# Kernel tuning notes

Hardware: AMD Instinct MI355X
Metric: run time of the kernel (lower is better)

Reference implementation:

```python
import jax, jax.numpy as jnp
import numpy as np

KS = 3
N = KS ** 3  # 27 kernel sample points


def conv3d(x, w, b=None, pad=1):
    out = jax.lax.conv_general_dilated(
        x, w, (1, 1, 1), [(pad, pad)] * 3,
        dimension_numbers=('NCDHW', 'OIDHW', 'NCDHW'))
    if b is not None:
        out = out + b[None, :, None, None, None]
    return out


def batchnorm(x, g, b, eps=1e-5):
    # training-mode BN: batch statistics over (N,D,H,W), biased variance (torch default)
    m = x.mean(axis=(0, 2, 3, 4), keepdims=True)
    v = x.var(axis=(0, 2, 3, 4), keepdims=True)
    return (x - m) * jax.lax.rsqrt(v + eps) * g[None, :, None, None, None] + b[None, :, None, None, None]


def deform_conv3d(x, offset, w, pad=1):
    # x: (b,c,D,H,W); offset: (b,3N,D,H,W) channel order [d-offsets | h-offsets | w-offsets]
    b, c, D, H, W = x.shape
    xp = jnp.pad(x, ((0, 0), (0, 0), (pad, pad), (pad, pad), (pad, pad)))
    Dp, Hp, Wp = D + 2 * pad, H + 2 * pad, W + 2 * pad
    dt = offset.dtype
    r = (jnp.arange(KS) - (KS - 1) // 2).astype(dt)
    pn = jnp.stack(jnp.meshgrid(r, r, r, indexing='ij'), -1).reshape(N, 3)  # kernel grid offsets
    base = jnp.stack(jnp.meshgrid(jnp.arange(D) + pad, jnp.arange(H) + pad,
                                  jnp.arange(W) + pad, indexing='ij'), -1).astype(dt)  # (D,H,W,3)
    off = jnp.transpose(offset.reshape(b, 3, N, D, H, W), (0, 3, 4, 5, 2, 1))  # (b,D,H,W,N,3)
    p = base[None, :, :, :, None, :] + pn[None, None, None, None] + off  # fractional sample coords
    dims = jnp.array([Dp, Hp, Wp], dtype=dt)
    q0 = jnp.floor(p)
    q0c = jnp.clip(q0, 0, dims - 1)
    q1c = jnp.clip(q0 + 1, 0, dims - 1)
    pc = jnp.clip(p, 0, dims - 1)
    wlo = 1.0 + (q0c - pc)  # per-axis trilinear weight, low corner
    whi = 1.0 - (q1c - pc)  # per-axis trilinear weight, high corner
    q0i = q0c.astype(jnp.int32)
    q1i = q1c.astype(jnp.int32)
    xpf = xp.reshape(b, c, -1)
    M = D * H * W * N
    acc = jnp.zeros((b, c, D, H, W, N), dtype=x.dtype)
    for corner in range(8):  # fixed 8 trilinear corners
        sel = [(corner >> a) & 1 for a in range(3)]
        q = [q1i[..., a] if sel[a] else q0i[..., a] for a in range(3)]
        g = (whi[..., 0] if sel[0] else wlo[..., 0]) \
            * (whi[..., 1] if sel[1] else wlo[..., 1]) \
            * (whi[..., 2] if sel[2] else wlo[..., 2])
        idx = (q[0] * Hp + q[1]) * Wp + q[2]  # (b,D,H,W,N) flat gather index
        vals = jnp.take_along_axis(
            xpf, jnp.broadcast_to(idx.reshape(b, 1, M), (b, c, M)), axis=2
        ).reshape(b, c, D, H, W, N)
        acc = acc + g[:, None] * vals
    # kernel-stride-KS conv over the reshaped blocks == contraction over (c, N)
    outc = w.shape[0]
    return jnp.einsum('bcdhwn,ocn->bodhw', acc, w.reshape(outc, c, N))


def setup_inputs():
    key = jax.random.key(0)
    ks = jax.random.split(key, 8)
    f32 = jnp.float32
    return {
        'x': jax.random.normal(ks[0], (16, 1, 28, 28, 28), f32),
        'off_w': jax.random.normal(ks[1], (81, 1, 3, 3, 3), f32) * 0.05,
        'off_b': jnp.zeros((81,), f32),
        'dconv_w': jax.random.normal(ks[2], (32, 1, 3, 3, 3), f32) * 0.2,
        'bn1_g': jnp.ones((32,), f32), 'bn1_b': jnp.zeros((32,), f32),
        'conv2_w': jax.random.normal(ks[3], (64, 32, 3, 3, 3), f32) * 0.06,
        'conv2_b': jnp.zeros((64,), f32),
        'bn2_g': jnp.ones((64,), f32), 'bn2_b': jnp.zeros((64,), f32),
        'conv3_w': jax.random.normal(ks[4], (128, 64, 3, 3, 3), f32) * 0.04,
        'conv3_b': jnp.zeros((128,), f32),
        'bn3_g': jnp.ones((128,), f32), 'bn3_b': jnp.zeros((128,), f32),
        'conv4_w': jax.random.normal(ks[5], (128, 128, 3, 3, 3), f32) * 0.03,
        'conv4_b': jnp.zeros((128,), f32),
        'bn4_g': jnp.ones((128,), f32), 'bn4_b': jnp.zeros((128,), f32),
        'fc_w': jax.random.normal(ks[6], (10, 128), f32) * 0.1,
        'fc_b': jnp.zeros((10,), f32),
    }


def reference(x, off_w, off_b, dconv_w, bn1_g, bn1_b, conv2_w, conv2_b, bn2_g, bn2_b,
              conv3_w, conv3_b, bn3_g, bn3_b, conv4_w, conv4_b, bn4_g, bn4_b, fc_w, fc_b):
    offsets = conv3d(x, off_w, off_b)  # (b,81,D,H,W)
    h = batchnorm(jax.nn.relu(deform_conv3d(x, offsets, dconv_w)), bn1_g, bn1_b)
    h = batchnorm(jax.nn.relu(conv3d(h, conv2_w, conv2_b)), bn2_g, bn2_b)
    h = batchnorm(jax.nn.relu(conv3d(h, conv3_w, conv3_b)), bn3_g, bn3_b)
    h = batchnorm(jax.nn.relu(conv3d(h, conv4_w, conv4_b)), bn4_g, bn4_b)
    h = h.mean(axis=(2, 3, 4))  # avg_pool3d over full (28,28,d) -> (b,128)
    logits = h @ fc_w.T + fc_b
    return jax.nn.log_softmax(logits, axis=1), offsets
```

## Files before the change

kernel.cpp:

```cpp
#include <hip/hip_runtime.h>
#include <math.h>

#define Sv 21952
#define HWc 784
#define CNT 351232.0f
#define EPS 1e-5f
#define PV 27000
#define PT (16 * PV)

typedef short bf16x8 __attribute__((ext_vector_type(8)));
typedef float f32x4 __attribute__((ext_vector_type(4)));
typedef float f32x16 __attribute__((ext_vector_type(16)));
typedef unsigned short u16x8 __attribute__((ext_vector_type(8)));

__device__ __forceinline__ unsigned short f2bf(float f) {
    unsigned u = __float_as_uint(f);
    u = (u + 0x7FFFu + ((u >> 16) & 1u)) >> 16;
    return (unsigned short)u;
}
__device__ __forceinline__ float bf2f(unsigned short h) {
    return __uint_as_float(((unsigned)h) << 16);
}

__device__ __forceinline__ void async16(const unsigned short* g, unsigned short* l) {
    __builtin_amdgcn_global_load_lds(
        (const __attribute__((address_space(1))) unsigned int*)g,
        (__attribute__((address_space(3))) unsigned int*)l, 16, 0, 0);
}

__global__ __launch_bounds__(256) void k_offsets(const float* __restrict__ x,
        const float* __restrict__ ow, const float* __restrict__ ob,
        float* __restrict__ out) {
    __shared__ float w_s[81 * 27];
    __shared__ float b_s[81];
    for (int i = threadIdx.x; i < 81 * 27; i += 256) w_s[i] = ow[i];
    if (threadIdx.x < 81) b_s[threadIdx.x] = ob[threadIdx.x];
    __syncthreads();
    int idx = blockIdx.x * 256 + threadIdx.x;
    int n = idx / Sv, s = idx % Sv;
    int d = s / HWc, r = s % HWc, h = r / 28, w = r % 28;
    const float* xb = x + (long)n * Sv;
    float xv[27];
    #pragma unroll
    for (int dz = 0; dz < 3; dz++)
      #pragma unroll
      for (int dy = 0; dy < 3; dy++)
        #pragma unroll
        for (int dx = 0; dx < 3; dx++) {
            int zz = d + dz - 1, yy = h + dy - 1, xx = w + dx - 1;
            bool ok = (unsigned)zz < 28u && (unsigned)yy < 28u && (unsigned)xx < 28u;
            xv[dz * 9 + dy * 3 + dx] = ok ? xb[zz * HWc + yy * 28 + xx] : 0.f;
        }
    float* op = out + (long)n * 81 * Sv + s;
    for (int c = 0; c < 81; c++) {
        float acc = b_s[c];
        #pragma unroll
        for (int k = 0; k < 27; k++) acc += xv[k] * w_s[c * 27 + k];
        op[(long)c * Sv] = acc;
    }
}

__device__ __forceinline__ float fetch_pad(const float* __restrict__ xb,
                                           int zq, int yq, int xq) {
    int z = zq - 1, y = yq - 1, xx = xq - 1;
    bool ok = (unsigned)z < 28u && (unsigned)y < 28u && (unsigned)xx < 28u;
    return ok ? xb[z * HWc + y * 28 + xx] : 0.f;
}

__global__ __launch_bounds__(256) void k_deform(const float* __restrict__ x,
        const float* __restrict__ off, const float* __restrict__ dw,
        unsigned short* __restrict__ h1p) {
    __shared__ float w_s[32 * 27];
    for (int i = threadIdx.x; i < 32 * 27; i += 256) w_s[i] = dw[i];
    __syncthreads();
    int idx = blockIdx.x * 256 + threadIdx.x;
    int n = idx / Sv, s = idx % Sv;
    int d = s / HWc, r = s % HWc, h = r / 28, w = r % 28;
    const float* xb = x + (long)n * Sv;
    const float* ofb = off + (long)n * 81 * Sv + s;
    float v[27];
    #pragma unroll
    for (int k = 0; k < 27; k++) {
        int ki = k / 9, kj = (k / 3) % 3, kl = k % 3;
        float pd = (float)(d + ki) + ofb[(long)k * Sv];
        float ph = (float)(h + kj) + ofb[(long)(27 + k) * Sv];
        float pw = (float)(w + kl) + ofb[(long)(54 + k) * Sv];
        float q0d = floorf(pd), q0h = floorf(ph), q0w = floorf(pw);
        float pcd = fminf(fmaxf(pd, 0.f), 29.f);
        float pch = fminf(fmaxf(ph, 0.f), 29.f);
        float pcw = fminf(fmaxf(pw, 0.f), 29.f);
        float q0cd = fminf(fmaxf(q0d, 0.f), 29.f);
        float q0ch = fminf(fmaxf(q0h, 0.f), 29.f);
        float q0cw = fminf(fmaxf(q0w, 0.f), 29.f);
        float q1cd = fminf(fmaxf(q0d + 1.f, 0.f), 29.f);
        float q1ch = fminf(fmaxf(q0h + 1.f, 0.f), 29.f);
        float q1cw = fminf(fmaxf(q0w + 1.f, 0.f), 29.f);
        float wz[2] = {1.f + (q0cd - pcd), 1.f - (q1cd - pcd)};
        float wy[2] = {1.f + (q0ch - pch), 1.f - (q1ch - pch)};
        float wx[2] = {1.f + (q0cw - pcw), 1.f - (q1cw - pcw)};
        int qz[2] = {(int)q0cd, (int)q1cd};
        int qy[2] = {(int)q0ch, (int)q1ch};
        int qx[2] = {(int)q0cw, (int)q1cw};
        float val = 0.f;
        #pragma unroll
        for (int cz = 0; cz < 2; cz++)
          #pragma unroll
          for (int cy = 0; cy < 2; cy++)
            #pragma unroll
            for (int cx = 0; cx < 2; cx++)
                val += wz[cz] * wy[cy] * wx[cx] * fetch_pad(xb, qz[cz], qy[cy], qx[cx]);
        v[k] = val;
    }
    unsigned pb = ((((unsigned)n * 30 + (d + 1)) * 30 + (h + 1)) * 30 + (w + 1)) * 32;
    unsigned short tmp[32];
    #pragma unroll
    for (int o = 0; o < 32; o++) {
        float acc = 0.f;
        #pragma unroll
        for (int k = 0; k < 27; k++) acc += v[k] * w_s[o * 27 + k];
        tmp[o] = f2bf(fmaxf(acc, 0.f));
    }
    u16x8* dst = (u16x8*)(h1p + pb);
    #pragma unroll
    for (int q = 0; q < 4; q++) dst[q] = ((u16x8*)tmp)[q];
}

template<int C>
__global__ __launch_bounds__(256) void k_stats_p(const unsigned short* __restrict__ buf,
        float* __restrict__ sums) {
    constexpr int G = C / 8;
    constexpr int P = 256 / G;
    int t = threadIdx.x;
    int oct = t % G, ps = t / G;
    float s1[8], s2[8];
    #pragma unroll
    for (int j = 0; j < 8; j++) { s1[j] = 0.f; s2[j] = 0.f; }
    for (int p = blockIdx.x * P + ps; p < PT; p += gridDim.x * P) {
        u16x8 v = *(const u16x8*)(buf + (long)p * C + oct * 8);
        #pragma unroll
        for (int j = 0; j < 8; j++) {
            float f = bf2f(v[j]);
            s1[j] += f; s2[j] += f * f;
        }
    }
    __shared__ float sh[2][C];
    if (t < C) { sh[0][t] = 0.f; sh[1][t] = 0.f; }
    __syncthreads();
    #pragma unroll
    for (int j = 0; j < 8; j++) {
        atomicAdd(&sh[0][oct * 8 + j], s1[j]);
        atomicAdd(&sh[1][oct * 8 + j], s2[j]);
    }
    __syncthreads();
    if (t < C) { atomicAdd(&sums[t], sh[0][t]); atomicAdd(&sums[C + t], sh[1][t]); }
}

__global__ void k_finalize(const float* __restrict__ sums, const float* __restrict__ g,
        const float* __restrict__ bb, float* __restrict__ aff, int C) {
    int c = threadIdx.x;
    if (c < C) {
        float mean = sums[c] * (1.f / CNT);
        float var = sums[C + c] * (1.f / CNT) - mean * mean;
        float a = g[c] * rsqrtf(var + EPS);
        aff[c] = a;
        aff[C + c] = bb[c] - mean * a;
    }
}

template<int CI, int COT>
__global__ __launch_bounds__(256) void k_wfrag32(const float* __restrict__ w,
        const float* __restrict__ affa, unsigned short* __restrict__ wf) {
    constexpr int NT32 = COT / 32;
    constexpr int KC = CI / 32;
    int tid = blockIdx.x * 256 + threadIdx.x;
    int lane = tid & 63, rest = tid >> 6;
    int kh = rest & 1; rest >>= 1;
    int nt = rest % NT32; rest /= NT32;
    int kc = rest % KC;
    int tap = rest / KC;
    if (tap >= 27) return;
    int co = nt * 32 + (lane & 31);
    int hi = lane >> 5;
    unsigned short tmp[8];
    #pragma unroll
    for (int j = 0; j < 8; j++) {
        int ci = kc * 32 + kh * 16 + hi * 8 + j;
        tmp[j] = f2bf(w[((long)co * CI + ci) * 27 + tap] * affa[ci]);
    }
    long oidx = ((((long)kc * 27 + tap) * NT32 + nt) * 2 + kh) * 512 + lane * 8;
    *(u16x8*)(wf + oidx) = *(u16x8*)tmp;
}

template<int CI, int COT>
__global__ __launch_bounds__(256) void k_tapsum(const float* __restrict__ w,
        const float* __restrict__ affb, float* __restrict__ S) {
    __shared__ float acc[27];
    int co = blockIdx.x;
    int t = threadIdx.x;
    if (t < 27) acc[t] = 0.f;
    __syncthreads();
    const float* wr = w + (long)co * CI * 27;
    for (int idx = t; idx < CI * 27; idx += 256)
        atomicAdd(&acc[idx % 27], wr[idx] * affb[idx / 27]);
    __syncthreads();
    if (t < 27) S[t * COT + co] = acc[t];
}

template<int COT>
__global__ void k_btab2(const float* __restrict__ S, const float* __restrict__ bias,
        float* __restrict__ T) {
    int tid = blockIdx.x * 256 + threadIdx.x;
    if (tid >= 27 * COT) return;
    int co = tid % COT, cls = tid / COT;
    int xc = cls % 3, yc = (cls / 3) % 3, zc = cls / 9;
    float val = bias[co];
    #pragma unroll
    for (int t = 0; t < 27; t++) {
        int dx = t % 3, dy = (t / 3) % 3, dz = t / 9;
        bool ok = (zc == 1 || (zc == 0 && dz >= 1) || (zc == 2 && dz <= 1))
               && (yc == 1 || (yc == 0 && dy >= 1) || (yc == 2 && dy <= 1))
               && (xc == 1 || (xc == 0 && dx >= 1) || (xc == 2 && dx <= 1));
        if (ok) val += S[t * COT + co];
    }
    T[cls * COT + co] = val;
}

template<int CI, int COT, int WN, bool PAD_OUT>
__global__ __launch_bounds__(WN * 128, 2) void k_conv_mfma(
        const unsigned short* __restrict__ in,
        const unsigned short* __restrict__ wfrag,
        const float* __restrict__ Ttab,
        unsigned short* __restrict__ out) {
    constexpr int KC = CI / 32;
    constexpr int NT32 = COT / 32;
    constexpr int NW = WN * 2;
    constexpr int NTW = (NW >= 4) ? NT32 / 2 : NT32;
    constexpr int NT = WN * 128;
    constexpr int CP = 720;
    constexpr int CUU = CP * 5;
    constexpr int NLOAD = (CUU + NT - 1) / NT;
    constexpr int LDSU = CUU + 48;
    __shared__ unsigned short lds[LDSU * 8];

    int tid = threadIdx.x, wv = tid >> 6, lane = tid & 63;
    int lcol = lane & 31, hi = lane >> 5;
    int wv_m = wv & 1, wv_n = wv >> 1;

    int bx = blockIdx.x;
    int xcd = bx & 7, loc = bx >> 3;
    int n = xcd * 2 + loc / 98;
    int rem = loc % 98;
    int z0 = (rem / 7) * 2;
    int y0 = (rem % 7) * 4;
    const unsigned short* src = in + ((long)((n * 30 + z0) * 30 + y0) * 30) * CI;

    int baseA[4];
    #pragma unroll
    for (int mt = 0; mt < 4; mt++) {
        int x = lcol; if (x > 27) x = 27;
        int pos = (wv_m * 6 + mt) * 30 + x;
        baseA[mt] = pos * 80 + hi * 16;
    }

    f32x16 acc[4][NTW];
    #pragma unroll
    for (int mt = 0; mt < 4; mt++)
        #pragma unroll
        for (int nt = 0; nt < NTW; nt++)
            #pragma unroll
            for (int e = 0; e < 16; e++) acc[mt][nt][e] = 0.f;

    for (int kc = 0; kc < KC; kc++) {
        if (kc) __syncthreads();
        #pragma unroll
        for (int j = 0; j < NLOAD; j++) {
            int wb = j * NT + (wv << 6);
            if (wb < CUU) {
                int u = wb + lane;
                if (u >= CUU) u = CUU - 1;
                int p = u / 5, s = u - p * 5;
                int q = s & 3;
                int zl = p / 180, r = p - zl * 180;
                int yl = r / 30, xl = r - yl * 30;
                int so = (zl * 900 + yl * 30 + xl) * CI + q * 8 + kc * 32;
                async16(src + so, lds + (wb << 3));
            }
        }
        __syncthreads();
        const unsigned short* pwk =
            wfrag + (long)(kc * 27) * NT32 * 1024 + (long)wv_n * (NTW * 1024)
                  + lane * 8;
        bf16x8 bc[NTW][2];
        #pragma unroll
        for (int nt = 0; nt < NTW; nt++)
            #pragma unroll
            for (int kh = 0; kh < 2; kh++)
                bc[nt][kh] = *(const bf16x8*)(pwk + nt * 1024 + kh * 512);
        #pragma unroll
        for (int tap = 0; tap < 27; tap++) {
            int td = (((tap / 9) * 6 + (tap % 9) / 3) * 30 + tap % 3) * 80;
            bf16x8 bn[NTW][2];
            if (tap < 26) {
                const unsigned short* pwn = pwk + (long)(tap + 1) * NT32 * 1024;
                #pragma unroll
                for (int nt = 0; nt < NTW; nt++)
                    #pragma unroll
                    for (int kh = 0; kh < 2; kh++)
                        bn[nt][kh] = *(const bf16x8*)(pwn + nt * 1024 + kh * 512);
            }
            bf16x8 a[2][4];
            #pragma unroll
            for (int kh = 0; kh < 2; kh++)
                #pragma unroll
                for (int mt = 0; mt < 4; mt++)
                    a[kh][mt] = *(const bf16x8*)((const char*)lds
                                 + baseA[mt] + td + kh * 32);
            #pragma unroll
            for (int kh = 0; kh < 2; kh++)
                #pragma unroll
                for (int mt = 0; mt < 4; mt++)
                    #pragma unroll
                    for (int nt = 0; nt < NTW; nt++)
                        acc[mt][nt] = __builtin_amdgcn_mfma_f32_32x32x16_bf16(
                            a[kh][mt], bc[nt][kh], acc[mt][nt], 0, 0, 0);
            if (tap < 26) {
                #pragma unroll
                for (int nt = 0; nt < NTW; nt++)
                    #pragma unroll
                    for (int kh = 0; kh < 2; kh++)
                        bc[nt][kh] = bn[nt][kh];
            }
        }
    }

    int zz = z0 + wv_m;
    int zc = (zz == 0) ? 0 : ((zz == 27) ? 2 : 1);
    #pragma unroll
    for (int mt = 0; mt < 4; mt++) {
        int y = y0 + mt;
        int yc = (y == 0) ? 0 : ((y == 27) ? 2 : 1);
        #pragma unroll
        for (int reg = 0; reg < 16; reg++) {
            int x = (reg & 3) + 8 * (reg >> 2) + 4 * hi;
            if (x >= 28) continue;
            int xc = (x == 0) ? 0 : ((x == 27) ? 2 : 1);
            int cls = (zc * 3 + yc) * 3 + xc;
            long ob;
            if (PAD_OUT)
                ob = ((long)((n * 30 + zz + 1) * 30 + y + 1) * 30 + x + 1) * COT;
            else
                ob = ((long)n * Sv + zz * HWc + y * 28 + x) * COT;
            #pragma unroll
            for (int nt = 0; nt < NTW; nt++) {
                int co = wv_n * (NTW * 32) + nt * 32 + lcol;
                float v = acc[mt][nt][reg] + Ttab[cls * COT + co];
                out[ob + co] = f2bf(fmaxf(v, 0.f));
            }
        }
    }
}

__global__ __launch_bounds__(256) void k_stats4(const unsigned short* __restrict__ h4,
        float* __restrict__ pooled, float* __restrict__ chsq) {
    int n = blockIdx.x, zs = blockIdx.y;
    int t = threadIdx.x;
    int oct = t % 16, ps = t / 16;
    long base = (long)n * Sv + zs * HWc;
    float s1[8], s2[8];
    #pragma unroll
    for (int j = 0; j < 8; j++) { s1[j] = 0.f; s2[j] = 0.f; }
    for (int p = ps; p < HWc; p += 16) {
        u16x8 v = *(const u16x8*)(h4 + (base + p) * 128 + oct * 8);
        #pragma unroll
        for (int j = 0; j < 8; j++) {
            float f = bf2f(v[j]);
            s1[j] += f; s2[j] += f * f;
        }
    }
    __shared__ float sh[2][128];
    if (t < 128) { sh[0][t] = 0.f; sh[1][t] = 0.f; }
    __syncthreads();
    #pragma unroll
    for (int j = 0; j < 8; j++) {
        atomicAdd(&sh[0][oct * 8 + j], s1[j]);
        atomicAdd(&sh[1][oct * 8 + j], s2[j]);
    }
    __syncthreads();
    if (t < 128) {
        atomicAdd(&pooled[n * 128 + t], sh[0][t]);
        atomicAdd(&chsq[t], sh[1][t]);
    }
}

__global__ __launch_bounds__(256) void k_head(const float* __restrict__ pooled,
        const float* __restrict__ chsq, const float* __restrict__ g4,
        const float* __restrict__ b4, const float* __restrict__ fcw,
        const float* __restrict__ fcb, float* __restrict__ out) {
    __shared__ float feat[16 * 128];
    __shared__ float lg[160];
    __shared__ float corr[16];
    int t = threadIdx.x;
    if (t < 128) {
        float sum = 0.f;
        for (int n = 0; n < 16; n++) sum += pooled[n * 128 + t];
        float mean = sum * (1.f / CNT);
        float var = chsq[t] * (1.f / CNT) - mean * mean;
        float a = g4[t] * rsqrtf(var + EPS);
        float bb = b4[t] - mean * a;
        for (int n = 0; n < 16; n++)
            feat[n * 128 + t] = a * (pooled[n * 128 + t] * (1.f / (float)Sv)) + bb;
    }
    __syncthreads();
    if (t < 160) {
        int n = t / 10, j = t % 10;
        float acc = fcb[j];
        for (int c = 0; c < 128; c++) acc += feat[n * 128 + c] * fcw[j * 128 + c];
        lg[t] = acc;
    }
    __syncthreads();
    if (t < 16) {
        float mx = -1e30f;
        for (int j = 0; j < 10; j++) mx = fmaxf(mx, lg[t * 10 + j]);
        float se = 0.f;
        for (int j = 0; j < 10; j++) se += expf(lg[t * 10 + j] - mx);
        corr[t] = mx + logf(se);
    }
    __syncthreads();
    if (t < 160) out[t] = lg[t] - corr[t / 10];
}

#define OFF_H3P 0L
#define OFF_H2P 110592000L
#define OFF_H1P 165888000L
#define OFF_H4  110592000L
#define OFF_WF2 200507392L
#define OFF_WF3 200617984L
#define OFF_WF4 201060352L
#define OFF_STATS 201945088L

extern "C" void kernel_launch(void* const* d_in, const int* in_sizes, int n_in,
                              void* d_out, int out_size, void* d_ws, size_t ws_size,
                              hipStream_t stream) {
    const float* x       = (const float*)d_in[0];
    const float* off_w   = (const float*)d_in[1];
    const float* off_b   = (const float*)d_in[2];
    const float* dconv_w = (const float*)d_in[3];
    const float* bn1_g   = (const float*)d_in[4];
    const float* bn1_b   = (const float*)d_in[5];
    const float* conv2_w = (const float*)d_in[6];
    const float* conv2_b = (const float*)d_in[7];
    const float* bn2_g   = (const float*)d_in[8];
    const float* bn2_b   = (const float*)d_in[9];
    const float* conv3_w = (const float*)d_in[10];
    const float* conv3_b = (const float*)d_in[11];
    const float* bn3_g   = (const float*)d_in[12];
    const float* bn3_b   = (const float*)d_in[13];
    const float* conv4_w = (const float*)d_in[14];
    const float* conv4_b = (const float*)d_in[15];
    const float* bn4_g   = (const float*)d_in[16];
    const float* bn4_b   = (const float*)d_in[17];
    const float* fc_w    = (const float*)d_in[18];
    const float* fc_b    = (const float*)d_in[19];

    float* out = (float*)d_out;
    float* offsets = out + 160;

    char* ws = (char*)d_ws;
    unsigned short* h3p = (unsigned short*)(ws + OFF_H3P);
    unsigned short* h2p = (unsigned short*)(ws + OFF_H2P);
    unsigned short* h1p = (unsigned short*)(ws + OFF_H1P);
    unsigned short* h4  = (unsigned short*)(ws + OFF_H4);
    unsigned short* wf2 = (unsigned short*)(ws + OFF_WF2);
    unsigned short* wf3 = (unsigned short*)(ws + OFF_WF3);
    unsigned short* wf4 = (unsigned short*)(ws + OFF_WF4);
    float* st = (float*)(ws + OFF_STATS);
    float* sums1 = st;        float* aff1 = st + 64;
    float* sums2 = st + 128;  float* aff2 = st + 256;
    float* sums3 = st + 384;  float* aff3 = st + 640;
    float* chsq4 = st + 896;  float* pooled = st + 1024;
    float* T2 = st + 4096;    float* T3 = st + 8192;   float* T4 = st + 16384;
    float* Sb = st + 20480;

    hipMemsetAsync(st, 0, 3072 * sizeof(float), stream);
    hipMemsetAsync(h1p, 0, 27648000L, stream);
    hipMemsetAsync(h2p, 0, 55296000L, stream);
    hipMemsetAsync(h3p, 0, 110592000L, stream);

    k_offsets<<<dim3(1372), 256, 0, stream>>>(x, off_w, off_b, offsets);
    k_deform<<<dim3(1372), 256, 0, stream>>>(x, offsets, dconv_w, h1p);

    k_stats_p<32><<<dim3(432), 256, 0, stream>>>(h1p, sums1);
    k_finalize<<<1, 32, 0, stream>>>(sums1, bn1_g, bn1_b, aff1, 32);
    k_wfrag32<32, 64><<<dim3(27), 256, 0, stream>>>(conv2_w, aff1, wf2);
    k_tapsum<32, 64><<<dim3(64), 256, 0, stream>>>(conv2_w, aff1 + 32, Sb);
    k_btab2<64><<<dim3(7), 256, 0, stream>>>(Sb, conv2_b, T2);
    k_conv_mfma<32, 64, 2, true><<<dim3(1568), 256, 0, stream>>>(h1p, wf2, T2, h2p);

    k_stats_p<64><<<dim3(432), 256, 0, stream>>>(h2p, sums2);
    k_finalize<<<1, 64, 0, stream>>>(sums2, bn2_g, bn2_b, aff2, 64);
    k_wfrag32<64, 128><<<dim3(108), 256, 0, stream>>>(conv3_w, aff2, wf3);
    k_tapsum<64, 128><<<dim3(128), 256, 0, stream>>>(conv3_w, aff2 + 64, Sb);
    k_btab2<128><<<dim3(14), 256, 0, stream>>>(Sb, conv3_b, T3);
    k_conv_mfma<64, 128, 2, true><<<dim3(1568), 256, 0, stream>>>(h2p, wf3, T3, h3p);

    k_stats_p<128><<<dim3(432), 256, 0, stream>>>(h3p, sums3);
    k_finalize<<<1, 128, 0, stream>>>(sums3, bn3_g, bn3_b, aff3, 128);
    k_wfrag32<128, 128><<<dim3(216), 256, 0, stream>>>(conv4_w, aff3, wf4);
    k_tapsum<128, 128><<<dim3(128), 256, 0, stream>>>(conv4_w, aff3 + 128, Sb);
    k_btab2<128><<<dim3(14), 256, 0, stream>>>(Sb, conv4_b, T4);
    k_conv_mfma<128, 128, 2, false><<<dim3(1568), 256, 0, stream>>>(h3p, wf4, T4, h4);

    k_stats4<<<dim3(16, 28), 256, 0, stream>>>(h4, pooled, chsq4);
    k_head<<<1, 256, 0, stream>>>(pooled, chsq4, bn4_g, bn4_b, fc_w, fc_b, out);
}
```

Before: 1.134 ms.

## Fuse batchnorm statistics into producer kernels and drop final activation store

Per-channel sum and sum-of-squares for each batchnorm are now accumulated in the epilogues of the deform and MFMA conv kernels, via shared-memory atomics followed by global atomics, replacing separate stats kernels. This removes a full re-read of each bf16 activation buffer. The last conv no longer writes its output at all: it reduces straight into the pooled and squared-sum buffers, skipping the h4 store and read. The cost is shared-memory atomic contention in the epilogues, notably per-output atomics in the deform kernel.

```diff
diff --git a/kernel.cpp b/kernel.cpp
--- a/kernel.cpp
+++ b/kernel.cpp
@@ -69,9 +69,11 @@
 
 __global__ __launch_bounds__(256) void k_deform(const float* __restrict__ x,
         const float* __restrict__ off, const float* __restrict__ dw,
-        unsigned short* __restrict__ h1p) {
+        unsigned short* __restrict__ h1p, float* __restrict__ sums) {
     __shared__ float w_s[32 * 27];
+    __shared__ float sh[2][32];
     for (int i = threadIdx.x; i < 32 * 27; i += 256) w_s[i] = dw[i];
+    if (threadIdx.x < 32) { sh[0][threadIdx.x] = 0.f; sh[1][threadIdx.x] = 0.f; }
     __syncthreads();
     int idx = blockIdx.x * 256 + threadIdx.x;
     int n = idx / Sv, s = idx % Sv;
@@ -118,41 +120,20 @@
         float acc = 0.f;
         #pragma unroll
         for (int k = 0; k < 27; k++) acc += v[k] * w_s[o * 27 + k];
-        tmp[o] = f2bf(fmaxf(acc, 0.f));
+        unsigned short hb = f2bf(fmaxf(acc, 0.f));
+        tmp[o] = hb;
+        float vr = bf2f(hb);
+        atomicAdd(&sh[0][o], vr);
+        atomicAdd(&sh[1][o], vr * vr);
     }
     u16x8* dst = (u16x8*)(h1p + pb);
     #pragma unroll
     for (int q = 0; q < 4; q++) dst[q] = ((u16x8*)tmp)[q];
-}
-
-template<int C>
-__global__ __launch_bounds__(256) void k_stats_p(const unsigned short* __restrict__ buf,
-        float* __restrict__ sums) {
-    constexpr int G = C / 8;
-    constexpr int P = 256 / G;
-    int t = threadIdx.x;
-    int oct = t % G, ps = t / G;
-    float s1[8], s2[8];
-    #pragma unroll
-    for (int j = 0; j < 8; j++) { s1[j] = 0.f; s2[j] = 0.f; }
-    for (int p = blockIdx.x * P + ps; p < PT; p += gridDim.x * P) {
-        u16x8 v = *(const u16x8*)(buf + (long)p * C + oct * 8);
-        #pragma unroll
-        for (int j = 0; j < 8; j++) {
-            float f = bf2f(v[j]);
-            s1[j] += f; s2[j] += f * f;
-        }
-    }
-    __shared__ float sh[2][C];
-    if (t < C) { sh[0][t] = 0.f; sh[1][t] = 0.f; }
-    __syncthreads();
-    #pragma unroll
-    for (int j = 0; j < 8; j++) {
-        atomicAdd(&sh[0][oct * 8 + j], s1[j]);
-        atomicAdd(&sh[1][oct * 8 + j], s2[j]);
-    }
-    __syncthreads();
-    if (t < C) { atomicAdd(&sums[t], sh[0][t]); atomicAdd(&sums[C + t], sh[1][t]); }
+    __syncthreads();
+    if (threadIdx.x < 32) {
+        atomicAdd(&sums[threadIdx.x], sh[0][threadIdx.x]);
+        atomicAdd(&sums[32 + threadIdx.x], sh[1][threadIdx.x]);
+    }
 }
 
 __global__ void k_finalize(const float* __restrict__ sums, const float* __restrict__ g,
@@ -225,26 +206,28 @@
     T[cls * COT + co] = val;
 }
 
-template<int CI, int COT, int WN, bool PAD_OUT>
+template<int CI, int COT, int WN, bool PAD_OUT, int SMODE>
 __global__ __launch_bounds__(WN * 128, 2) void k_conv_mfma(
         const unsigned short* __restrict__ in,
         const unsigned short* __restrict__ wfrag,
         const float* __restrict__ Ttab,
-        unsigned short* __restrict__ out) {
+        unsigned short* __restrict__ out,
+        float* __restrict__ sa, float* __restrict__ sb) {
     constexpr int KC = CI / 32;
     constexpr int NT32 = COT / 32;
-    constexpr int NW = WN * 2;
-    constexpr int NTW = (NW >= 4) ? NT32 / 2 : NT32;
+    constexpr int NTW = NT32 / 2;
     constexpr int NT = WN * 128;
     constexpr int CP = 720;
     constexpr int CUU = CP * 5;
     constexpr int NLOAD = (CUU + NT - 1) / NT;
     constexpr int LDSU = CUU + 48;
     __shared__ unsigned short lds[LDSU * 8];
+    __shared__ float shs[2][COT];
 
     int tid = threadIdx.x, wv = tid >> 6, lane = tid & 63;
     int lcol = lane & 31, hi = lane >> 5;
     int wv_m = wv & 1, wv_n = wv >> 1;
+    if (tid < COT) { shs[0][tid] = 0.f; shs[1][tid] = 0.f; }
 
     int bx = blockIdx.x;
     int xcd = bx & 7, loc = bx >> 3;
@@ -335,6 +318,9 @@
 
     int zz = z0 + wv_m;
     int zc = (zz == 0) ? 0 : ((zz == 27) ? 2 : 1);
+    float s1a[NTW], s2a[NTW];
+    #pragma unroll
+    for (int nt = 0; nt < NTW; nt++) { s1a[nt] = 0.f; s2a[nt] = 0.f; }
     #pragma unroll
     for (int mt = 0; mt < 4; mt++) {
         int y = y0 + mt;
@@ -345,50 +331,39 @@
             if (x >= 28) continue;
             int xc = (x == 0) ? 0 : ((x == 27) ? 2 : 1);
             int cls = (zc * 3 + yc) * 3 + xc;
-            long ob;
-            if (PAD_OUT)
-                ob = ((long)((n * 30 + zz + 1) * 30 + y + 1) * 30 + x + 1) * COT;
-            else
-                ob = ((long)n * Sv + zz * HWc + y * 28 + x) * COT;
+            long ob = 0;
+            if constexpr (SMODE == 0) {
+                if (PAD_OUT)
+                    ob = ((long)((n * 30 + zz + 1) * 30 + y + 1) * 30 + x + 1) * COT;
+                else
+                    ob = ((long)n * Sv + zz * HWc + y * 28 + x) * COT;
+            }
             #pragma unroll
             for (int nt = 0; nt < NTW; nt++) {
                 int co = wv_n * (NTW * 32) + nt * 32 + lcol;
                 float v = acc[mt][nt][reg] + Ttab[cls * COT + co];
-                out[ob + co] = f2bf(fmaxf(v, 0.f));
+                unsigned short hb = f2bf(fmaxf(v, 0.f));
+                if constexpr (SMODE == 0) out[ob + co] = hb;
+                float vr = bf2f(hb);
+                s1a[nt] += vr;
+                s2a[nt] += vr * vr;
             }
         }
     }
-}
-
-__global__ __launch_bounds__(256) void k_stats4(const unsigned short* __restrict__ h4,
-        float* __restrict__ pooled, float* __restrict__ chsq) {
-    int n = blockIdx.x, zs = blockIdx.y;
-    int t = threadIdx.x;
-    int oct = t % 16, ps = t / 16;
-    long base = (long)n * Sv + zs * HWc;
-    float s1[8], s2[8];
-    #pragma unroll
-    for (int j = 0; j < 8; j++) { s1[j] = 0.f; s2[j] = 0.f; }
-    for (int p = ps; p < HWc; p += 16) {
-        u16x8 v = *(const u16x8*)(h4 + (base + p) * 128 + oct * 8);
-        #pragma unroll
-        for (int j = 0; j < 8; j++) {
-            float f = bf2f(v[j]);
-            s1[j] += f; s2[j] += f * f;
+    #pragma unroll
+    for (int nt = 0; nt < NTW; nt++) {
+        int co = wv_n * (NTW * 32) + nt * 32 + lcol;
+        atomicAdd(&shs[0][co], s1a[nt]);
+        atomicAdd(&shs[1][co], s2a[nt]);
+    }
+    __syncthreads();
+    if (tid < COT) {
+        if constexpr (SMODE == 1) {
+            atomicAdd(&sa[n * COT + tid], shs[0][tid]);
+        } else {
+            atomicAdd(&sa[tid], shs[0][tid]);
         }
-    }
-    __shared__ float sh[2][128];
-    if (t < 128) { sh[0][t] = 0.f; sh[1][t] = 0.f; }
-    __syncthreads();
-    #pragma unroll
-    for (int j = 0; j < 8; j++) {
-        atomicAdd(&sh[0][oct * 8 + j], s1[j]);
-        atomicAdd(&sh[1][oct * 8 + j], s2[j]);
-    }
-    __syncthreads();
-    if (t < 128) {
-        atomicAdd(&pooled[n * 128 + t], sh[0][t]);
-        atomicAdd(&chsq[t], sh[1][t]);
+        atomicAdd(&sb[tid], shs[1][tid]);
     }
 }
 
@@ -432,7 +407,6 @@
 #define OFF_H3P 0L
 #define OFF_H2P 110592000L
 #define OFF_H1P 165888000L
-#define OFF_H4  110592000L
 #define OFF_WF2 200507392L
 #define OFF_WF3 200617984L
 #define OFF_WF4 201060352L
@@ -469,7 +443,6 @@
     unsigned short* h3p = (unsigned short*)(ws + OFF_H3P);
     unsigned short* h2p = (unsigned short*)(ws + OFF_H2P);
     unsigned short* h1p = (unsigned short*)(ws + OFF_H1P);
-    unsigned short* h4  = (unsigned short*)(ws + OFF_H4);
     unsigned short* wf2 = (unsigned short*)(ws + OFF_WF2);
     unsigned short* wf3 = (unsigned short*)(ws + OFF_WF3);
     unsigned short* wf4 = (unsigned short*)(ws + OFF_WF4);
@@ -487,29 +460,28 @@
     hipMemsetAsync(h3p, 0, 110592000L, stream);
 
     k_offsets<<<dim3(1372), 256, 0, stream>>>(x, off_w, off_b, offsets);
-    k_deform<<<dim3(1372), 256, 0, stream>>>(x, offsets, dconv_w, h1p);
-
-    k_stats_p<32><<<dim3(432), 256, 0, stream>>>(h1p, sums1);
+    k_deform<<<dim3(1372), 256, 0, stream>>>(x, offsets, dconv_w, h1p, sums1);
+
     k_finalize<<<1, 32, 0, stream>>>(sums1, bn1_g, bn1_b, aff1, 32);
     k_wfrag32<32, 64><<<dim3(27), 256, 0, stream>>>(conv2_w, aff1, wf2);
     k_tapsum<32, 64><<<dim3(64), 256, 0, stream>>>(conv2_w, aff1 + 32, Sb);
     k_btab2<64><<<dim3(7), 256, 0, stream>>>(Sb, conv2_b, T2);
-    k_conv_mfma<32, 64, 2, true><<<dim3(1568), 256, 0, stream>>>(h1p, wf2, T2, h2p);
-
-    k_stats_p<64><<<dim3(432), 256, 0, stream>>>(h2p, sums2);
+    k_conv_mfma<32, 64, 2, true, 0><<<dim3(1568), 256, 0, stream>>>(
+        h1p, wf2, T2, h2p, sums2, sums2 + 64);
+
     k_finalize<<<1, 64, 0, stream>>>(sums2, bn2_g, bn2_b, aff2, 64);
     k_wfrag32<64, 128><<<dim3(108), 256, 0, stream>>>(conv3_w, aff2, wf3);
     k_tapsum<64, 128><<<dim3(128), 256, 0, stream>>>(conv3_w, aff2 + 64, Sb);
     k_btab2<128><<<dim3(14), 256, 0, stream>>>(Sb, conv3_b, T3);
-    k_conv_mfma<64, 128, 2, true><<<dim3(1568), 256, 0, stream>>>(h2p, wf3, T3, h3p);
-
-    k_stats_p<128><<<dim3(432), 256, 0, stream>>>(h3p, sums3);
+    k_conv_mfma<64, 128, 2, true, 0><<<dim3(1568), 256, 0, stream>>>(
+        h2p, wf3, T3, h3p, sums3, sums3 + 128);
+
     k_finalize<<<1, 128, 0, stream>>>(sums3, bn3_g, bn3_b, aff3, 128);
     k_wfrag32<128, 128><<<dim3(216), 256, 0, stream>>>(conv4_w, aff3, wf4);
     k_tapsum<128, 128><<<dim3(128), 256, 0, stream>>>(conv4_w, aff3 + 128, Sb);
     k_btab2<128><<<dim3(14), 256, 0, stream>>>(Sb, conv4_b, T4);
-    k_conv_mfma<128, 128, 2, false><<<dim3(1568), 256, 0, stream>>>(h3p, wf4, T4, h4);
-
-    k_stats4<<<dim3(16, 28), 256, 0, stream>>>(h4, pooled, chsq4);
+    k_conv_mfma<128, 128, 2, false, 1><<<dim3(1568), 256, 0, stream>>>(
+        h3p, wf4, T4, (unsigned short*)0, pooled, chsq4);
+
     k_head<<<1, 256, 0, stream>>>(pooled, chsq4, bn4_g, bn4_b, fc_w, fc_b, out);
 }
```

Measured after the change: 1.717 ms. 1.51x slower.
